# Optimization experiments

Hardware: AMD Instinct MI355X
Metric: run time of the kernel (lower is better)

Reference implementation:

```python
import jax, jax.numpy as jnp
import numpy as np


def fake_quant(w, bits):
    # Symmetric per-tensor fake quantization with straight-through estimator.
    qmax = 2.0 ** (bits - 1) - 1.0
    scale = jnp.max(jnp.abs(w)) / qmax
    wq = jnp.clip(jnp.round(w / scale), -qmax, qmax) * scale
    return w + jax.lax.stop_gradient(wq - w)


def setup_inputs() -> dict:
    key = jax.random.key(0)
    k = jax.random.split(key, 5)
    B, S, D, H = 64, 196, 768, 3072
    x = jax.random.normal(k[0], (B, S, D), dtype=jnp.float32)
    w1 = jax.random.normal(k[1], (H, D), dtype=jnp.float32) * (1.0 / np.sqrt(D))
    b1 = jax.random.normal(k[2], (H,), dtype=jnp.float32) * 0.01
    w2 = jax.random.normal(k[3], (D, H), dtype=jnp.float32) * (1.0 / np.sqrt(H))
    b2 = jax.random.normal(k[4], (D,), dtype=jnp.float32) * 0.01
    return {"x": x, "w1": w1, "b1": b1, "w2": w2, "b2": b2, "bits": 8}


def reference(x, w1, b1, w2, b2, bits):
    # fc1 (fake-quant weight) -> ReLU -> fc2 (fake-quant weight)
    w1q = fake_quant(w1, bits)
    w2q = fake_quant(w2, bits)
    h = jnp.einsum('bsd,hd->bsh', x, w1q) + b1   # [B,S,3072]
    h = jax.nn.relu(h)
    out = jnp.einsum('bsh,dh->bsd', h, w2q) + b2  # [B,S,768]
    return out
```

## Files before the change

kernel.cpp:

```cpp
#include <hip/hip_runtime.h>
#include <hip/hip_bf16.h>
#include <stdint.h>

typedef __attribute__((ext_vector_type(8))) short bf16x8;
typedef __attribute__((ext_vector_type(4))) float f32x4;

__device__ __forceinline__ unsigned short f2bf(float f) {
  __hip_bfloat16 h = __float2bfloat16(f);
  return *reinterpret_cast<unsigned short*>(&h);
}

__global__ void absmax_kernel(const float* __restrict__ w, int n4,
                              unsigned int* __restrict__ out) {
  __shared__ unsigned int red[256];
  unsigned int m = 0u;
  const uint4* w4 = reinterpret_cast<const uint4*>(w);
  for (int i = blockIdx.x * blockDim.x + threadIdx.x; i < n4;
       i += gridDim.x * blockDim.x) {
    uint4 v = w4[i];
    m = max(m, v.x & 0x7fffffffu);
    m = max(m, v.y & 0x7fffffffu);
    m = max(m, v.z & 0x7fffffffu);
    m = max(m, v.w & 0x7fffffffu);
  }
  red[threadIdx.x] = m;
  __syncthreads();
  for (int s = 128; s > 0; s >>= 1) {
    if ((int)threadIdx.x < s)
      red[threadIdx.x] = max(red[threadIdx.x], red[threadIdx.x + s]);
    __syncthreads();
  }
  if (threadIdx.x == 0) atomicMax(out, red[0]);
}

__global__ void quant_kernel(const float* __restrict__ w, int n4,
                             const unsigned int* __restrict__ maxbits,
                             const int* __restrict__ bits,
                             unsigned short* __restrict__ out) {
  const float qmax = (float)((1 << (*bits - 1)) - 1);
  const float scale = __uint_as_float(*maxbits) / qmax;
  const float4* w4 = reinterpret_cast<const float4*>(w);
  ushort4* o4 = reinterpret_cast<ushort4*>(out);
  for (int i = blockIdx.x * blockDim.x + threadIdx.x; i < n4;
       i += gridDim.x * blockDim.x) {
    float4 v = w4[i];
    float a = fminf(fmaxf(rintf(v.x / scale), -qmax), qmax) * scale;
    float b = fminf(fmaxf(rintf(v.y / scale), -qmax), qmax) * scale;
    float c = fminf(fmaxf(rintf(v.z / scale), -qmax), qmax) * scale;
    float d = fminf(fmaxf(rintf(v.w / scale), -qmax), qmax) * scale;
    o4[i] = make_ushort4(f2bf(a), f2bf(b), f2bf(c), f2bf(d));
  }
}

__global__ void cast_kernel(const float* __restrict__ x, int n4,
                            unsigned short* __restrict__ out) {
  const float4* x4 = reinterpret_cast<const float4*>(x);
  ushort4* o4 = reinterpret_cast<ushort4*>(out);
  for (int i = blockIdx.x * blockDim.x + threadIdx.x; i < n4;
       i += gridDim.x * blockDim.x) {
    float4 v = x4[i];
    o4[i] = make_ushort4(f2bf(v.x), f2bf(v.y), f2bf(v.z), f2bf(v.w));
  }
}

template<int BM, bool RELU, bool BF16_OUT>
__global__ __launch_bounds__(256)
void gemm_bt(const unsigned short* __restrict__ A,
             const unsigned short* __restrict__ B,
             const float* __restrict__ bias,
             void* __restrict__ Cout,
             int M, int N, int K, int gx) {
  constexpr int BK = 64;
  constexpr int MF = BM / 32;
  __shared__ __attribute__((aligned(16))) unsigned short As[BM * BK];
  __shared__ __attribute__((aligned(16))) unsigned short Bs[128 * BK];

  const int nwg = gridDim.x;
  const int orig = blockIdx.x;
  const int q = nwg >> 3, r = nwg & 7;
  const int xcd = orig & 7, cidx = orig >> 3;
  const int wgid = (xcd < r ? xcd * (q + 1) : r * (q + 1) + (xcd - r) * q) + cidx;
  const int bx = wgid % gx;
  const int by = wgid / gx;

  const int tid = threadIdx.x;
  const int lane = tid & 63;
  const int wave = tid >> 6;
  const int wr = wave >> 1;
  const int wc = wave & 1;
  const long brow = (long)by * BM;
  const long bcol = (long)bx * 128;

  f32x4 acc[MF][4] = {};

  const int srow = lane >> 3;
  const int gslot = ((lane & 7) ^ (lane >> 3)) * 8;
  const int fr = lane & 15;
  const int fs = lane >> 4;

  for (int k0 = 0; k0 < K; k0 += BK) {
#pragma unroll
    for (int it = 0; it < BM / 32; ++it) {
      const int c = it * 4 + wave;
      const unsigned short* ga = A + (brow + c * 8 + srow) * (long)K + k0 + gslot;
      __builtin_amdgcn_global_load_lds(
          (const __attribute__((address_space(1))) void*)ga,
          (__attribute__((address_space(3))) void*)(As + c * 512), 16, 0, 0);
    }
#pragma unroll
    for (int it = 0; it < 4; ++it) {
      const int c = it * 4 + wave;
      const unsigned short* gb = B + (bcol + c * 8 + srow) * (long)K + k0 + gslot;
      __builtin_amdgcn_global_load_lds(
          (const __attribute__((address_space(1))) void*)gb,
          (__attribute__((address_space(3))) void*)(Bs + c * 512), 16, 0, 0);
    }
    __syncthreads();

#pragma unroll
    for (int kk = 0; kk < 2; ++kk) {
      const int s = kk * 4 + fs;
      bf16x8 a[MF], b[4];
#pragma unroll
      for (int m = 0; m < MF; ++m) {
        const int row = wr * (MF * 16) + m * 16 + fr;
        a[m] = *reinterpret_cast<const bf16x8*>(As + row * BK + ((s ^ (row & 7)) * 8));
      }
#pragma unroll
      for (int n = 0; n < 4; ++n) {
        const int row = wc * 64 + n * 16 + fr;
        b[n] = *reinterpret_cast<const bf16x8*>(Bs + row * BK + ((s ^ (row & 7)) * 8));
      }
#pragma unroll
      for (int m = 0; m < MF; ++m)
#pragma unroll
        for (int n = 0; n < 4; ++n)
          acc[m][n] = __builtin_amdgcn_mfma_f32_16x16x32_bf16(a[m], b[n], acc[m][n], 0, 0, 0);
    }
    __syncthreads();
  }

  const int fq = lane >> 4;
#pragma unroll
  for (int n = 0; n < 4; ++n) {
    const long col = bcol + wc * 64 + n * 16 + fr;
    const float bv = bias[col];
#pragma unroll
    for (int m = 0; m < MF; ++m) {
#pragma unroll
      for (int rr = 0; rr < 4; ++rr) {
        const long row = brow + wr * (MF * 16) + m * 16 + fq * 4 + rr;
        float v = acc[m][n][rr] + bv;
        if (RELU) v = fmaxf(v, 0.0f);
        if (BF16_OUT)
          ((unsigned short*)Cout)[row * N + col] = f2bf(v);
        else
          ((float*)Cout)[row * N + col] = v;
      }
    }
  }
}

extern "C" void kernel_launch(void* const* d_in, const int* in_sizes, int n_in,
                              void* d_out, int out_size, void* d_ws, size_t ws_size,
                              hipStream_t stream) {
  const float* x  = (const float*)d_in[0];
  const float* w1 = (const float*)d_in[1];
  const float* b1 = (const float*)d_in[2];
  const float* w2 = (const float*)d_in[3];
  const float* b2 = (const float*)d_in[4];
  const int* bits = (const int*)d_in[5];

  const int M = 64 * 196;
  const int D = 768, H = 3072;
  const int nx = M * D;
  const int nw1 = H * D;
  const int nw2 = D * H;

  char* ws = (char*)d_ws;
  unsigned int* scales = (unsigned int*)ws;
  unsigned short* xb  = (unsigned short*)(ws + 256);
  unsigned short* w1q = (unsigned short*)(ws + 256 + (size_t)nx * 2);
  unsigned short* w2q = (unsigned short*)(ws + 256 + (size_t)nx * 2 + (size_t)nw1 * 2);
  unsigned short* hb  = (unsigned short*)(ws + 256 + (size_t)nx * 2 + (size_t)(nw1 + nw2) * 2);

  hipMemsetAsync(scales, 0, 8, stream);
  absmax_kernel<<<832, 256, 0, stream>>>(w1, nw1 / 4, scales + 0);
  absmax_kernel<<<832, 256, 0, stream>>>(w2, nw2 / 4, scales + 1);
  quant_kernel<<<832, 256, 0, stream>>>(w1, nw1 / 4, scales + 0, bits, w1q);
  quant_kernel<<<832, 256, 0, stream>>>(w2, nw2 / 4, scales + 1, bits, w2q);
  cast_kernel<<<2048, 256, 0, stream>>>(x, nx / 4, xb);

  gemm_bt<128, true, true><<<(H / 128) * (M / 128), 256, 0, stream>>>(
      xb, w1q, b1, hb, M, H, D, H / 128);
  gemm_bt<64, false, false><<<(D / 128) * (M / 64), 256, 0, stream>>>(
      hb, w2q, b2, d_out, M, D, H, D / 128);
}
```

Measured before the change: 212.1 us.

## Double-buffer GEMM LDS tiles and merge weight quant kernels

The GEMM now uses two LDS buffers. Global-to-LDS loads for tile t+2 are issued while tile t is computed, with explicit vmcnt waits in place of the full syncthreads stall. The per-weight absmax and quant kernels are merged into single launches with a 2D grid, cutting launch count. Doubling LDS per block may lower occupancy, and the hand-counted vmcnt values must match the number of outstanding loads per thread.

```diff
diff --git a/kernel.cpp b/kernel.cpp
--- a/kernel.cpp
+++ b/kernel.cpp
@@ -10,8 +10,9 @@
   return *reinterpret_cast<unsigned short*>(&h);
 }
 
-__global__ void absmax_kernel(const float* __restrict__ w, int n4,
-                              unsigned int* __restrict__ out) {
+__global__ void absmax2_kernel(const float* __restrict__ w1, const float* __restrict__ w2,
+                               int n4, unsigned int* __restrict__ out) {
+  const float* w = blockIdx.y ? w2 : w1;
   __shared__ unsigned int red[256];
   unsigned int m = 0u;
   const uint4* w4 = reinterpret_cast<const uint4*>(w);
@@ -30,17 +31,19 @@
       red[threadIdx.x] = max(red[threadIdx.x], red[threadIdx.x + s]);
     __syncthreads();
   }
-  if (threadIdx.x == 0) atomicMax(out, red[0]);
-}
-
-__global__ void quant_kernel(const float* __restrict__ w, int n4,
-                             const unsigned int* __restrict__ maxbits,
-                             const int* __restrict__ bits,
-                             unsigned short* __restrict__ out) {
+  if (threadIdx.x == 0) atomicMax(out + blockIdx.y, red[0]);
+}
+
+__global__ void quant2_kernel(const float* __restrict__ w1, const float* __restrict__ w2,
+                              int n4, const unsigned int* __restrict__ maxbits,
+                              const int* __restrict__ bits,
+                              unsigned short* __restrict__ o1, unsigned short* __restrict__ o2) {
+  const float* w = blockIdx.y ? w2 : w1;
+  unsigned short* o = blockIdx.y ? o2 : o1;
   const float qmax = (float)((1 << (*bits - 1)) - 1);
-  const float scale = __uint_as_float(*maxbits) / qmax;
+  const float scale = __uint_as_float(maxbits[blockIdx.y]) / qmax;
   const float4* w4 = reinterpret_cast<const float4*>(w);
-  ushort4* o4 = reinterpret_cast<ushort4*>(out);
+  ushort4* o4 = reinterpret_cast<ushort4*>(o);
   for (int i = blockIdx.x * blockDim.x + threadIdx.x; i < n4;
        i += gridDim.x * blockDim.x) {
     float4 v = w4[i];
@@ -72,8 +75,8 @@
              int M, int N, int K, int gx) {
   constexpr int BK = 64;
   constexpr int MF = BM / 32;
-  __shared__ __attribute__((aligned(16))) unsigned short As[BM * BK];
-  __shared__ __attribute__((aligned(16))) unsigned short Bs[128 * BK];
+  __shared__ __attribute__((aligned(16))) unsigned short As[2][BM * BK];
+  __shared__ __attribute__((aligned(16))) unsigned short Bs[2][128 * BK];
 
   const int nwg = gridDim.x;
   const int orig = blockIdx.x;
@@ -98,14 +101,14 @@
   const int fr = lane & 15;
   const int fs = lane >> 4;
 
-  for (int k0 = 0; k0 < K; k0 += BK) {
+  auto stage = [&](int k0, int b) {
 #pragma unroll
     for (int it = 0; it < BM / 32; ++it) {
       const int c = it * 4 + wave;
       const unsigned short* ga = A + (brow + c * 8 + srow) * (long)K + k0 + gslot;
       __builtin_amdgcn_global_load_lds(
           (const __attribute__((address_space(1))) void*)ga,
-          (__attribute__((address_space(3))) void*)(As + c * 512), 16, 0, 0);
+          (__attribute__((address_space(3))) void*)(&As[b][c * 512]), 16, 0, 0);
     }
 #pragma unroll
     for (int it = 0; it < 4; ++it) {
@@ -113,31 +116,51 @@
       const unsigned short* gb = B + (bcol + c * 8 + srow) * (long)K + k0 + gslot;
       __builtin_amdgcn_global_load_lds(
           (const __attribute__((address_space(1))) void*)gb,
-          (__attribute__((address_space(3))) void*)(Bs + c * 512), 16, 0, 0);
-    }
-    __syncthreads();
-
+          (__attribute__((address_space(3))) void*)(&Bs[b][c * 512]), 16, 0, 0);
+    }
+  };
+
+  const int nt = K / BK;
+  stage(0, 0);
+  stage(BK, 1);
+
+  for (int t = 0; t < nt; ++t) {
+    const int b = t & 1;
+    if (t < nt - 1) {
+      if constexpr (BM == 128) asm volatile("s_waitcnt vmcnt(8)" ::: "memory");
+      else                     asm volatile("s_waitcnt vmcnt(6)" ::: "memory");
+    } else {
+      asm volatile("s_waitcnt vmcnt(0)" ::: "memory");
+    }
+    __builtin_amdgcn_s_barrier();
+
+    const unsigned short* as = &As[b][0];
+    const unsigned short* bs = &Bs[b][0];
 #pragma unroll
     for (int kk = 0; kk < 2; ++kk) {
       const int s = kk * 4 + fs;
-      bf16x8 a[MF], b[4];
+      bf16x8 a[MF], bb[4];
 #pragma unroll
       for (int m = 0; m < MF; ++m) {
         const int row = wr * (MF * 16) + m * 16 + fr;
-        a[m] = *reinterpret_cast<const bf16x8*>(As + row * BK + ((s ^ (row & 7)) * 8));
+        a[m] = *reinterpret_cast<const bf16x8*>(as + row * BK + ((s ^ (row & 7)) * 8));
       }
 #pragma unroll
       for (int n = 0; n < 4; ++n) {
         const int row = wc * 64 + n * 16 + fr;
-        b[n] = *reinterpret_cast<const bf16x8*>(Bs + row * BK + ((s ^ (row & 7)) * 8));
+        bb[n] = *reinterpret_cast<const bf16x8*>(bs + row * BK + ((s ^ (row & 7)) * 8));
       }
 #pragma unroll
       for (int m = 0; m < MF; ++m)
 #pragma unroll
         for (int n = 0; n < 4; ++n)
-          acc[m][n] = __builtin_amdgcn_mfma_f32_16x16x32_bf16(a[m], b[n], acc[m][n], 0, 0, 0);
-    }
-    __syncthreads();
+          acc[m][n] = __builtin_amdgcn_mfma_f32_16x16x32_bf16(a[m], bb[n], acc[m][n], 0, 0, 0);
+    }
+
+    asm volatile("s_waitcnt lgkmcnt(0)" ::: "memory");
+    __builtin_amdgcn_sched_barrier(0);
+    __builtin_amdgcn_s_barrier();
+    if (t + 2 < nt) stage((t + 2) * BK, b);
   }
 
   const int fq = lane >> 4;
@@ -185,10 +208,8 @@
   unsigned short* hb  = (unsigned short*)(ws + 256 + (size_t)nx * 2 + (size_t)(nw1 + nw2) * 2);
 
   hipMemsetAsync(scales, 0, 8, stream);
-  absmax_kernel<<<832, 256, 0, stream>>>(w1, nw1 / 4, scales + 0);
-  absmax_kernel<<<832, 256, 0, stream>>>(w2, nw2 / 4, scales + 1);
-  quant_kernel<<<832, 256, 0, stream>>>(w1, nw1 / 4, scales + 0, bits, w1q);
-  quant_kernel<<<832, 256, 0, stream>>>(w2, nw2 / 4, scales + 1, bits, w2q);
+  absmax2_kernel<<<dim3(512, 2), 256, 0, stream>>>(w1, w2, nw1 / 4, scales);
+  quant2_kernel<<<dim3(512, 2), 256, 0, stream>>>(w1, w2, nw1 / 4, scales, bits, w1q, w2q);
   cast_kernel<<<2048, 256, 0, stream>>>(x, nx / 4, xb);
 
   gemm_bt<128, true, true><<<(H / 128) * (M / 128), 256, 0, stream>>>(
```

Result: faster. 197.3 us (-7.0%).
